# Performance work log

Measured on AMD Instinct MI355X. Metric: run time of the kernel, lower is better.

## Reference

```python
import jax, jax.numpy as jnp
import numpy as np

BATCH = 128
L = 4096
DIM = 64
N = 3   # rate-1/3 encoder: three 1-channel branches concatenated
EPS = 1e-3  # keras BatchNormalization default epsilon


def _bn(y, g, be, m, v):
    # inference-mode BatchNormalization over the channel (last) axis
    return g * (y - m) * jax.lax.rsqrt(v + EPS) + be


def _circ_unit(x, w, b, g, be, m, v):
    # Circular 'same' padding for kernel_size=5, stride=1 -> pad_window = 2
    xp = jnp.concatenate([x[:, -2:], x, x[:, :2]], axis=1)  # [B, L+4, C]
    y = jax.lax.conv_general_dilated(
        xp, w, window_strides=(1,), padding='VALID',
        dimension_numbers=('NWC', 'WIO', 'NWC')) + b        # [B, L, DIM]
    return jax.nn.elu(_bn(y, g, be, m, v))


def setup_inputs() -> dict:
    key = jax.random.key(0)
    ks = iter(jax.random.split(key, 16))

    def nrm(shape, s=0.05):
        return jax.random.normal(next(ks), shape, dtype=jnp.float32) * s

    inp = {}
    inp['x'] = jax.random.uniform(next(ks), (BATCH, L, 1), dtype=jnp.float32)
    # Pseudo_random_Interleaver: per-row permutation seeded by row index
    inp['perm'] = jnp.asarray(
        np.stack([np.random.RandomState(i).permutation(L) for i in range(BATCH)]),
        dtype=jnp.int32)
    for p in ('c1', 'c2', 'cI'):
        inp[p + '_w'] = nrm((5, 1, DIM)); inp[p + '_b'] = jnp.zeros((DIM,), jnp.float32)
        inp[p + '_g'] = jnp.ones((DIM,), jnp.float32); inp[p + '_be'] = jnp.zeros((DIM,), jnp.float32)
        inp[p + '_m'] = jnp.zeros((DIM,), jnp.float32); inp[p + '_v'] = jnp.ones((DIM,), jnp.float32)
    for p in ('f1', 'f2', 'fI'):
        inp[p + '_w'] = nrm((DIM, 1)); inp[p + '_b'] = jnp.zeros((1,), jnp.float32)
    inp['mp_w'] = nrm((1, DIM)); inp['mp_b'] = jnp.zeros((DIM,), jnp.float32)
    inp['mp_g'] = jnp.ones((DIM,), jnp.float32); inp['mp_be'] = jnp.zeros((DIM,), jnp.float32)
    inp['mp_m'] = jnp.zeros((DIM,), jnp.float32); inp['mp_v'] = jnp.ones((DIM,), jnp.float32)
    inp['md_w'] = nrm((DIM, 2)); inp['md_b'] = jnp.zeros((2,), jnp.float32)
    inp['md_g'] = jnp.ones((2,), jnp.float32); inp['md_be'] = jnp.zeros((2,), jnp.float32)
    inp['md_m'] = jnp.zeros((2,), jnp.float32); inp['md_v'] = jnp.ones((2,), jnp.float32)
    return inp


def reference(x, perm,
              c1_w, c1_b, c1_g, c1_be, c1_m, c1_v,
              c2_w, c2_b, c2_g, c2_be, c2_m, c2_v,
              cI_w, cI_b, cI_g, cI_be, cI_m, cI_v,
              f1_w, f1_b, f2_w, f2_b, fI_w, fI_b,
              mp_w, mp_b, mp_g, mp_be, mp_m, mp_v,
              md_w, md_b, md_g, md_be, md_m, md_v):
    x = 2.0 * x - 1.0  # bits -> +/-1
    # systematic branches
    e1 = jnp.einsum('bld,do->blo', _circ_unit(x, c1_w, c1_b, c1_g, c1_be, c1_m, c1_v), f1_w) + f1_b
    e2 = jnp.einsum('bld,do->blo', _circ_unit(x, c2_w, c2_b, c2_g, c2_be, c2_m, c2_v), f2_w) + f2_b
    # interleaved branch: one batched gather replaces the per-sample python loop
    xI = jnp.take_along_axis(x, perm[:, :, None], axis=1)
    eI = jnp.einsum('bld,do->blo', _circ_unit(xI, cI_w, cI_b, cI_g, cI_be, cI_m, cI_v), fI_w) + fI_b
    y = jnp.concatenate([e1, e2, eI], axis=-1)          # [B, L, 3]
    yt = y.reshape(BATCH, L * N, 1)                     # k = 1
    # Modulation: 1x1 conv (elu) then 1x1 conv to 2 coords (linear), each with BN
    mo = jax.nn.elu(_bn(jnp.einsum('blk,kd->bld', yt, mp_w) + mp_b, mp_g, mp_be, mp_m, mp_v))
    coord = _bn(jnp.einsum('bld,dc->blc', mo, md_w) + md_b, md_g, md_be, md_m, md_v)
    return coord  # [B, 3L, 2]
```

## Files before the change

### kernel.cpp

```cpp
#include <hip/hip_runtime.h>
#include <math.h>

#define BATCH 128
#define LL    4096
#define DIM   64
#define EPS   1e-3f
#define LUTN  2048

#define LOG2E 1.44269504088896340736f
#define LN2   0.69314718055994530942f

#define GC2 0.2402265069591007f
#define GC3 0.05550410866482158f
#define GC4 0.009618129107628477f
#define GC5 0.0013333558146428443f


typedef float f32x2 __attribute__((ext_vector_type(2)));

__device__ __forceinline__ f32x2 pk_fma(f32x2 a, f32x2 b, f32x2 c) {
    return __builtin_elementwise_fma(a, b, c);
}

__device__ __forceinline__ float elu_plain(float z) {
    return z > 0.0f ? z : (__expf(z) - 1.0f);
}

__global__ __launch_bounds__(256) void enc_prep(
    const float* __restrict__ cw0, const float* __restrict__ cb0, const float* __restrict__ cg0,
    const float* __restrict__ cbe0, const float* __restrict__ cm0, const float* __restrict__ cv0,
    const float* __restrict__ cw1, const float* __restrict__ cb1, const float* __restrict__ cg1,
    const float* __restrict__ cbe1, const float* __restrict__ cm1, const float* __restrict__ cv1,
    const float* __restrict__ cw2, const float* __restrict__ cb2, const float* __restrict__ cg2,
    const float* __restrict__ cbe2, const float* __restrict__ cm2, const float* __restrict__ cv2,
    const float* __restrict__ f0w, const float* __restrict__ f0b,
    const float* __restrict__ f1w, const float* __restrict__ f1b,
    const float* __restrict__ f2w, const float* __restrict__ f2b,
    const float* __restrict__ mpw, const float* __restrict__ mpb, const float* __restrict__ mpg,
    const float* __restrict__ mpbe, const float* __restrict__ mpm, const float* __restrict__ mpv,
    const float* __restrict__ mdw, const float* __restrict__ mdb, const float* __restrict__ mdg,
    const float* __restrict__ mdbe, const float* __restrict__ mdm, const float* __restrict__ mdv,
    float* __restrict__ W)
{
    const int t   = threadIdx.x;
    const int blk = blockIdx.x;
    __shared__ float smod[64][4];
    __shared__ float s_lo[3], s_hi[3];
    __shared__ float sD[2];
    __shared__ float srange[2];

    if (t < 192) {
        const int br = t >> 6;
        const int d  = t & 63;
        const float* cw  = (br == 0) ? cw0  : (br == 1) ? cw1  : cw2;
        const float* cb  = (br == 0) ? cb0  : (br == 1) ? cb1  : cb2;
        const float* cg  = (br == 0) ? cg0  : (br == 1) ? cg1  : cg2;
        const float* cbe = (br == 0) ? cbe0 : (br == 1) ? cbe1 : cbe2;
        const float* cm  = (br == 0) ? cm0  : (br == 1) ? cm1  : cm2;
        const float* cv  = (br == 0) ? cv0  : (br == 1) ? cv1  : cv2;
        const float* fw  = (br == 0) ? f0w  : (br == 1) ? f1w  : f2w;
        const float s = cg[d] / sqrtf(cv[d] + EPS);
        float tap[5], habs = 0.0f;
        #pragma unroll
        for (int k = 0; k < 5; ++k) {
            tap[k] = cw[k * 64 + d] * s * LOG2E;
            habs += fabsf(tap[k]);
        }
        const float bias = ((cb[d] - cm[d]) * s + cbe[d]) * LOG2E;
        const float fwd  = fw[d];
        if (blk == 0) {
            float* o = W + ((d >> 1) * 3 + br) * 16 + (d & 1);
            o[0] = tap[0]; o[2] = tap[1]; o[4] = tap[2]; o[6] = tap[3]; o[8] = tap[4];
            o[10] = bias; o[12] = fwd;
        }
        const float hb = LN2 * (habs + fabsf(bias));
        float r0 = fwd * tap[0], r1 = fwd * tap[1], r2 = fwd * tap[2];
        float r3 = fwd * tap[3], r4 = fwd * tap[4], rb = fwd * bias;
        float myS = fabsf(fwd) * fmaxf(1.0f, hb);
        #pragma unroll
        for (int off = 32; off; off >>= 1) {
            r0 += __shfl_down(r0, off);
            r1 += __shfl_down(r1, off);
            r2 += __shfl_down(r2, off);
            r3 += __shfl_down(r3, off);
            r4 += __shfl_down(r4, off);
            rb += __shfl_down(rb, off);
            myS += __shfl_down(myS, off);
        }
        if ((t & 63) == 0) {
            const float fb = ((br == 0) ? f0b : (br == 1) ? f1b : f2b)[0];
            s_lo[br] = fb - myS;
            s_hi[br] = fb + myS;
            if (blk == 0) {
                float* Lb = W + 1536 + br * 8;
                Lb[0] = LN2 * r0; Lb[1] = LN2 * r1; Lb[2] = LN2 * r2;
                Lb[3] = LN2 * r3; Lb[4] = LN2 * r4; Lb[5] = LN2 * rb;
                W[1560 + br] = fb;
            }
        }
    } else {
        const int d = t - 192;
        const float smp = mpg[d] / sqrtf(mpv[d] + EPS);
        const float A = mpw[d] * smp;
        const float C = (mpb[d] - mpm[d]) * smp + mpbe[d];
        const float s0 = mdg[0] / sqrtf(mdv[0] + EPS);
        const float s1 = mdg[1] / sqrtf(mdv[1] + EPS);
        smod[d][0] = A;
        smod[d][1] = C;
        smod[d][2] = mdw[d * 2 + 0] * s0;
        smod[d][3] = mdw[d * 2 + 1] * s1;
        if (d == 0) {
            const float D0 = (mdb[0] - mdm[0]) * s0 + mdbe[0];
            const float D1 = (mdb[1] - mdm[1]) * s1 + mdbe[1];
            sD[0] = D0; sD[1] = D1;
            if (blk == 0) { W[1563] = D0; W[1564] = D1; }
        }
    }
    __syncthreads();

    if (t == 0) {
        float lo = fminf(s_lo[0], fminf(s_lo[1], s_lo[2]));
        float hi = fmaxf(s_hi[0], fmaxf(s_hi[1], s_hi[2]));
        float pad = 1e-3f * (hi - lo) + 1e-6f;
        lo -= pad; hi += pad;
        srange[0] = lo;
        srange[1] = (hi - lo) / (float)(LUTN - 1);
        if (blk == 0) {
            const float invh = (float)(LUTN - 1) / (hi - lo);
            W[1565] = invh;
            W[1566] = -lo * invh;
            W[1567] = lo;
        }
    }
    __syncthreads();

    const int i = blk * 256 + t;
    const float lo = srange[0], hs = srange[1];
    const float D0 = sD[0], D1 = sD[1];
    const float e0 = fmaf((float)i, hs, lo);
    const float e1 = fmaf((float)(i + 1), hs, lo);
    float a0 = D0, a1 = D1, b0 = D0, b1 = D1;
    #pragma unroll 8
    for (int d = 0; d < 64; ++d) {
        const float A = smod[d][0], C = smod[d][1], m0 = smod[d][2], m1 = smod[d][3];
        float u;
        u = elu_plain(fmaf(A, e0, C)); a0 = fmaf(m0, u, a0); a1 = fmaf(m1, u, a1);
        u = elu_plain(fmaf(A, e1, C)); b0 = fmaf(m0, u, b0); b1 = fmaf(m1, u, b1);
    }
    float4* lut = (float4*)(W + 1568);
    lut[i] = make_float4(a0, a1, b0 - a0, b1 - a1);
}

__device__ __forceinline__ float2 lut_eval(float e, float invh, float nlo,
                                           const float4* __restrict__ lut) {
    float tt = fminf(fmaxf(fmaf(e, invh, nlo), 0.0f), (float)(LUTN - 1));
    float fi = floorf(tt); float f = tt - fi;
    float4 v = lut[(int)fi];
    return make_float2(fmaf(f, v.z, v.x), fmaf(f, v.w, v.y));
}

__device__ __forceinline__ void nl_acc(f32x2 h, f32x2 fw, f32x2& e) {
    const f32x2 zero = {0.0f, 0.0f};
    f32x2 z  = __builtin_elementwise_min(h, zero);
    f32x2 zz = z * z;
    f32x2 s  = pk_fma(z, f32x2{GC5, GC5}, f32x2{GC4, GC4});
    s = pk_fma(z, s, f32x2{GC3, GC3});
    s = pk_fma(z, s, f32x2{GC2, GC2});
    e = pk_fma(fw, zz * s, e);
}

__global__ __launch_bounds__(256) void enc_main(
    const float* __restrict__ x, const int* __restrict__ perm,
    const float* __restrict__ W, float* __restrict__ out)
{
    const int gid = blockIdx.x * 256 + threadIdx.x;
    const int b   = gid >> 11;
    const int l0  = (gid & (2048 - 1)) * 2;
    const float* xrow = x + ((size_t)b << 12);
    const int*   prow = perm + ((size_t)b << 12);

    const int ba = (l0 - 2) & (LL - 1);
    const int bc = (l0 + 2) & (LL - 1);
    const float2 w01 = *(const float2*)(xrow + ba);
    const float2 w23 = *(const float2*)(xrow + l0);
    const float2 w45 = *(const float2*)(xrow + bc);
    const int2 p01 = *(const int2*)(prow + ba);
    const int2 p23 = *(const int2*)(prow + l0);
    const int2 p45 = *(const int2*)(prow + bc);

    float xw[6], xg[6];
    xw[0] = fmaf(2.0f, w01.x, -1.0f); xw[1] = fmaf(2.0f, w01.y, -1.0f);
    xw[2] = fmaf(2.0f, w23.x, -1.0f); xw[3] = fmaf(2.0f, w23.y, -1.0f);
    xw[4] = fmaf(2.0f, w45.x, -1.0f); xw[5] = fmaf(2.0f, w45.y, -1.0f);
    xg[0] = fmaf(2.0f, xrow[p01.x], -1.0f); xg[1] = fmaf(2.0f, xrow[p01.y], -1.0f);
    xg[2] = fmaf(2.0f, xrow[p23.x], -1.0f); xg[3] = fmaf(2.0f, xrow[p23.y], -1.0f);
    xg[4] = fmaf(2.0f, xrow[p45.x], -1.0f); xg[5] = fmaf(2.0f, xrow[p45.y], -1.0f);

    f32x2 xs[6], xi[6];
    #pragma unroll
    for (int k = 0; k < 6; ++k) {
        xs[k] = f32x2{xw[k], xw[k]};
        xi[k] = f32x2{xg[k], xg[k]};
    }

    const float* LA = W + 1536;
    const float* LB = W + 1544;
    const float* LC = W + 1552;
    float linA0 = fmaf(LA[0], xw[0], fmaf(LA[1], xw[1], fmaf(LA[2], xw[2],
                  fmaf(LA[3], xw[3], fmaf(LA[4], xw[4], LA[5])))));
    float linA1 = fmaf(LA[0], xw[1], fmaf(LA[1], xw[2], fmaf(LA[2], xw[3],
                  fmaf(LA[3], xw[4], fmaf(LA[4], xw[5], LA[5])))));
    float linB0 = fmaf(LB[0], xw[0], fmaf(LB[1], xw[1], fmaf(LB[2], xw[2],
                  fmaf(LB[3], xw[3], fmaf(LB[4], xw[4], LB[5])))));
    float linB1 = fmaf(LB[0], xw[1], fmaf(LB[1], xw[2], fmaf(LB[2], xw[3],
                  fmaf(LB[3], xw[4], fmaf(LB[4], xw[5], LB[5])))));
    float linC0 = fmaf(LC[0], xg[0], fmaf(LC[1], xg[1], fmaf(LC[2], xg[2],
                  fmaf(LC[3], xg[3], fmaf(LC[4], xg[4], LC[5])))));
    float linC1 = fmaf(LC[0], xg[1], fmaf(LC[1], xg[2], fmaf(LC[2], xg[3],
                  fmaf(LC[3], xg[4], fmaf(LC[4], xg[5], LC[5])))));

    f32x2 eA0 = {0.0f, 0.0f}, eA1 = {0.0f, 0.0f};
    f32x2 eB0 = {0.0f, 0.0f}, eB1 = {0.0f, 0.0f};
    f32x2 eC0 = {0.0f, 0.0f}, eC1 = {0.0f, 0.0f};

    #pragma unroll 4
    for (int j = 0; j < 32; ++j) {
        const f32x2* tp = (const f32x2*)W + j * 24;
        f32x2 h;

        h = pk_fma(tp[0], xs[0], pk_fma(tp[1], xs[1], pk_fma(tp[2], xs[2],
            pk_fma(tp[3], xs[3], pk_fma(tp[4], xs[4], tp[5])))));
        nl_acc(h, tp[6], eA0);
        h = pk_fma(tp[0], xs[1], pk_fma(tp[1], xs[2], pk_fma(tp[2], xs[3],
            pk_fma(tp[3], xs[4], pk_fma(tp[4], xs[5], tp[5])))));
        nl_acc(h, tp[6], eA1);

        h = pk_fma(tp[8], xs[0], pk_fma(tp[9], xs[1], pk_fma(tp[10], xs[2],
            pk_fma(tp[11], xs[3], pk_fma(tp[12], xs[4], tp[13])))));
        nl_acc(h, tp[14], eB0);
        h = pk_fma(tp[8], xs[1], pk_fma(tp[9], xs[2], pk_fma(tp[10], xs[3],
            pk_fma(tp[11], xs[4], pk_fma(tp[12], xs[5], tp[13])))));
        nl_acc(h, tp[14], eB1);

        h = pk_fma(tp[16], xi[0], pk_fma(tp[17], xi[1], pk_fma(tp[18], xi[2],
            pk_fma(tp[19], xi[3], pk_fma(tp[20], xi[4], tp[21])))));
        nl_acc(h, tp[22], eC0);
        h = pk_fma(tp[16], xi[1], pk_fma(tp[17], xi[2], pk_fma(tp[18], xi[3],
            pk_fma(tp[19], xi[4], pk_fma(tp[20], xi[5], tp[21])))));
        nl_acc(h, tp[22], eC1);
    }

    const float fbA = W[1560], fbB = W[1561], fbC = W[1562];
    const float sA0 = fbA + linA0 + eA0.x + eA0.y;
    const float sA1 = fbA + linA1 + eA1.x + eA1.y;
    const float sB0 = fbB + linB0 + eB0.x + eB0.y;
    const float sB1 = fbB + linB1 + eB1.x + eB1.y;
    const float sC0 = fbC + linC0 + eC0.x + eC0.y;
    const float sC1 = fbC + linC1 + eC1.x + eC1.y;

    const float invh = W[1565], nlo = W[1566];
    const float4* lut = (const float4*)(W + 1568);
    float2 r0 = lut_eval(sA0, invh, nlo, lut);
    float2 r1 = lut_eval(sB0, invh, nlo, lut);
    float2 r2 = lut_eval(sC0, invh, nlo, lut);
    float2 r3 = lut_eval(sA1, invh, nlo, lut);
    float2 r4 = lut_eval(sB1, invh, nlo, lut);
    float2 r5 = lut_eval(sC1, invh, nlo, lut);

    float4* o4 = (float4*)(out + (size_t)gid * 12);
    o4[0] = make_float4(r0.x, r0.y, r1.x, r1.y);
    o4[1] = make_float4(r2.x, r2.y, r3.x, r3.y);
    o4[2] = make_float4(r4.x, r4.y, r5.x, r5.y);
}

extern "C" void kernel_launch(void* const* d_in, const int* in_sizes, int n_in,
                              void* d_out, int out_size, void* d_ws, size_t ws_size,
                              hipStream_t stream) {
    const float* x    = (const float*)d_in[0];
    const int*   perm = (const int*)d_in[1];
    float* W = (float*)d_ws;

    enc_prep<<<LUTN / 256, 256, 0, stream>>>(
        (const float*)d_in[2],  (const float*)d_in[3],  (const float*)d_in[4],
        (const float*)d_in[5],  (const float*)d_in[6],  (const float*)d_in[7],
        (const float*)d_in[8],  (const float*)d_in[9],  (const float*)d_in[10],
        (const float*)d_in[11], (const float*)d_in[12], (const float*)d_in[13],
        (const float*)d_in[14], (const float*)d_in[15], (const float*)d_in[16],
        (const float*)d_in[17], (const float*)d_in[18], (const float*)d_in[19],
        (const float*)d_in[20], (const float*)d_in[21],
        (const float*)d_in[22], (const float*)d_in[23],
        (const float*)d_in[24], (const float*)d_in[25],
        (const float*)d_in[26], (const float*)d_in[27], (const float*)d_in[28],
        (const float*)d_in[29], (const float*)d_in[30], (const float*)d_in[31],
        (const float*)d_in[32], (const float*)d_in[33], (const float*)d_in[34],
        (const float*)d_in[35], (const float*)d_in[36], (const float*)d_in[37],
        W);

    enc_main<<<(BATCH * LL) / 512, 256, 0, stream>>>(x, perm, W, (float*)d_out);
}
```

Before: 35.69 us.

## Process four positions per thread and fold x-to-bipolar mapping into weights

Each thread now computes four sequence positions instead of two. Weight loads from the workspace are amortized over twice as many conv and nonlinearity evaluations, and x/perm reads become float4/int4. The 2x-1 input transform is folded into the prepared taps, biases and linear terms, which removes the per-element FMA. The trade-off is higher register pressure, half as many threads and blocks (512 blocks), and the loop unroll dropping from 4 to 2.

```diff
diff --git a/kernel.cpp b/kernel.cpp
--- a/kernel.cpp
+++ b/kernel.cpp
@@ -60,18 +60,21 @@
         const float* cv  = (br == 0) ? cv0  : (br == 1) ? cv1  : cv2;
         const float* fw  = (br == 0) ? f0w  : (br == 1) ? f1w  : f2w;
         const float s = cg[d] / sqrtf(cv[d] + EPS);
-        float tap[5], habs = 0.0f;
+        float tap[5], habs = 0.0f, tsum = 0.0f;
         #pragma unroll
         for (int k = 0; k < 5; ++k) {
             tap[k] = cw[k * 64 + d] * s * LOG2E;
             habs += fabsf(tap[k]);
+            tsum += tap[k];
         }
         const float bias = ((cb[d] - cm[d]) * s + cbe[d]) * LOG2E;
         const float fwd  = fw[d];
         if (blk == 0) {
-            float* o = W + ((d >> 1) * 3 + br) * 16 + (d & 1);
-            o[0] = tap[0]; o[2] = tap[1]; o[4] = tap[2]; o[6] = tap[3]; o[8] = tap[4];
-            o[10] = bias; o[12] = fwd;
+            float* o = W + ((d >> 1) * 24 + br * 8) * 2 + (d & 1);
+            o[0] = 2.0f * tap[0]; o[2] = 2.0f * tap[1]; o[4] = 2.0f * tap[2];
+            o[6] = 2.0f * tap[3]; o[8] = 2.0f * tap[4];
+            o[10] = bias - tsum;
+            o[12] = fwd;
         }
         const float hb = LN2 * (habs + fabsf(bias));
         float r0 = fwd * tap[0], r1 = fwd * tap[1], r2 = fwd * tap[2];
@@ -93,8 +96,11 @@
             s_hi[br] = fb + myS;
             if (blk == 0) {
                 float* Lb = W + 1536 + br * 8;
-                Lb[0] = LN2 * r0; Lb[1] = LN2 * r1; Lb[2] = LN2 * r2;
-                Lb[3] = LN2 * r3; Lb[4] = LN2 * r4; Lb[5] = LN2 * rb;
+                const float rs = r0 + r1 + r2 + r3 + r4;
+                Lb[0] = 2.0f * LN2 * r0; Lb[1] = 2.0f * LN2 * r1;
+                Lb[2] = 2.0f * LN2 * r2; Lb[3] = 2.0f * LN2 * r3;
+                Lb[4] = 2.0f * LN2 * r4;
+                Lb[5] = LN2 * (rb - rs);
                 W[1560 + br] = fb;
             }
         }
@@ -169,108 +175,140 @@
     e = pk_fma(fw, zz * s, e);
 }
 
+#define CONV(tpb, xa, o) \
+    pk_fma(tpb[0], xa[o], pk_fma(tpb[1], xa[o+1], pk_fma(tpb[2], xa[o+2], \
+    pk_fma(tpb[3], xa[o+3], pk_fma(tpb[4], xa[o+4], tpb[5])))))
+
 __global__ __launch_bounds__(256) void enc_main(
     const float* __restrict__ x, const int* __restrict__ perm,
     const float* __restrict__ W, float* __restrict__ out)
 {
     const int gid = blockIdx.x * 256 + threadIdx.x;
-    const int b   = gid >> 11;
-    const int l0  = (gid & (2048 - 1)) * 2;
+    const int b   = gid >> 10;
+    const int l0  = (gid & 1023) * 4;
     const float* xrow = x + ((size_t)b << 12);
     const int*   prow = perm + ((size_t)b << 12);
 
-    const int ba = (l0 - 2) & (LL - 1);
-    const int bc = (l0 + 2) & (LL - 1);
-    const float2 w01 = *(const float2*)(xrow + ba);
-    const float2 w23 = *(const float2*)(xrow + l0);
-    const float2 w45 = *(const float2*)(xrow + bc);
-    const int2 p01 = *(const int2*)(prow + ba);
-    const int2 p23 = *(const int2*)(prow + l0);
-    const int2 p45 = *(const int2*)(prow + bc);
-
-    float xw[6], xg[6];
-    xw[0] = fmaf(2.0f, w01.x, -1.0f); xw[1] = fmaf(2.0f, w01.y, -1.0f);
-    xw[2] = fmaf(2.0f, w23.x, -1.0f); xw[3] = fmaf(2.0f, w23.y, -1.0f);
-    xw[4] = fmaf(2.0f, w45.x, -1.0f); xw[5] = fmaf(2.0f, w45.y, -1.0f);
-    xg[0] = fmaf(2.0f, xrow[p01.x], -1.0f); xg[1] = fmaf(2.0f, xrow[p01.y], -1.0f);
-    xg[2] = fmaf(2.0f, xrow[p23.x], -1.0f); xg[3] = fmaf(2.0f, xrow[p23.y], -1.0f);
-    xg[4] = fmaf(2.0f, xrow[p45.x], -1.0f); xg[5] = fmaf(2.0f, xrow[p45.y], -1.0f);
-
-    f32x2 xs[6], xi[6];
-    #pragma unroll
-    for (int k = 0; k < 6; ++k) {
-        xs[k] = f32x2{xw[k], xw[k]};
-        xi[k] = f32x2{xg[k], xg[k]};
-    }
+    const float4 q0 = *(const float4*)(xrow + ((l0 - 4) & (LL - 1)));
+    const float4 q1 = *(const float4*)(xrow + l0);
+    const float4 q2 = *(const float4*)(xrow + ((l0 + 4) & (LL - 1)));
+    const int4 pq0 = *(const int4*)(prow + ((l0 - 4) & (LL - 1)));
+    const int4 pq1 = *(const int4*)(prow + l0);
+    const int4 pq2 = *(const int4*)(prow + ((l0 + 4) & (LL - 1)));
+
+    float xw[8], xg[8];
+    xw[0] = q0.z; xw[1] = q0.w;
+    xw[2] = q1.x; xw[3] = q1.y; xw[4] = q1.z; xw[5] = q1.w;
+    xw[6] = q2.x; xw[7] = q2.y;
+    xg[0] = xrow[pq0.z]; xg[1] = xrow[pq0.w];
+    xg[2] = xrow[pq1.x]; xg[3] = xrow[pq1.y];
+    xg[4] = xrow[pq1.z]; xg[5] = xrow[pq1.w];
+    xg[6] = xrow[pq2.x]; xg[7] = xrow[pq2.y];
 
     const float* LA = W + 1536;
     const float* LB = W + 1544;
     const float* LC = W + 1552;
-    float linA0 = fmaf(LA[0], xw[0], fmaf(LA[1], xw[1], fmaf(LA[2], xw[2],
-                  fmaf(LA[3], xw[3], fmaf(LA[4], xw[4], LA[5])))));
-    float linA1 = fmaf(LA[0], xw[1], fmaf(LA[1], xw[2], fmaf(LA[2], xw[3],
-                  fmaf(LA[3], xw[4], fmaf(LA[4], xw[5], LA[5])))));
-    float linB0 = fmaf(LB[0], xw[0], fmaf(LB[1], xw[1], fmaf(LB[2], xw[2],
-                  fmaf(LB[3], xw[3], fmaf(LB[4], xw[4], LB[5])))));
-    float linB1 = fmaf(LB[0], xw[1], fmaf(LB[1], xw[2], fmaf(LB[2], xw[3],
-                  fmaf(LB[3], xw[4], fmaf(LB[4], xw[5], LB[5])))));
-    float linC0 = fmaf(LC[0], xg[0], fmaf(LC[1], xg[1], fmaf(LC[2], xg[2],
-                  fmaf(LC[3], xg[3], fmaf(LC[4], xg[4], LC[5])))));
-    float linC1 = fmaf(LC[0], xg[1], fmaf(LC[1], xg[2], fmaf(LC[2], xg[3],
-                  fmaf(LC[3], xg[4], fmaf(LC[4], xg[5], LC[5])))));
-
-    f32x2 eA0 = {0.0f, 0.0f}, eA1 = {0.0f, 0.0f};
-    f32x2 eB0 = {0.0f, 0.0f}, eB1 = {0.0f, 0.0f};
-    f32x2 eC0 = {0.0f, 0.0f}, eC1 = {0.0f, 0.0f};
-
-    #pragma unroll 4
+    f32x2 pw0[5], pw2[5], pg0[5], pg2[5];
+    #pragma unroll
+    for (int k = 0; k < 5; ++k) {
+        pw0[k] = f32x2{xw[k],     xw[k + 1]};
+        pw2[k] = f32x2{xw[k + 2], xw[k + 3]};
+        pg0[k] = f32x2{xg[k],     xg[k + 1]};
+        pg2[k] = f32x2{xg[k + 2], xg[k + 3]};
+    }
+    f32x2 linA01, linA23, linB01, linB23, linC01, linC23;
+    {
+        f32x2 la[6], lb[6], lc[6];
+        #pragma unroll
+        for (int k = 0; k < 6; ++k) {
+            la[k] = f32x2{LA[k], LA[k]};
+            lb[k] = f32x2{LB[k], LB[k]};
+            lc[k] = f32x2{LC[k], LC[k]};
+        }
+        linA01 = pk_fma(la[0], pw0[0], pk_fma(la[1], pw0[1], pk_fma(la[2], pw0[2],
+                 pk_fma(la[3], pw0[3], pk_fma(la[4], pw0[4], la[5])))));
+        linA23 = pk_fma(la[0], pw2[0], pk_fma(la[1], pw2[1], pk_fma(la[2], pw2[2],
+                 pk_fma(la[3], pw2[3], pk_fma(la[4], pw2[4], la[5])))));
+        linB01 = pk_fma(lb[0], pw0[0], pk_fma(lb[1], pw0[1], pk_fma(lb[2], pw0[2],
+                 pk_fma(lb[3], pw0[3], pk_fma(lb[4], pw0[4], lb[5])))));
+        linB23 = pk_fma(lb[0], pw2[0], pk_fma(lb[1], pw2[1], pk_fma(lb[2], pw2[2],
+                 pk_fma(lb[3], pw2[3], pk_fma(lb[4], pw2[4], lb[5])))));
+        linC01 = pk_fma(lc[0], pg0[0], pk_fma(lc[1], pg0[1], pk_fma(lc[2], pg0[2],
+                 pk_fma(lc[3], pg0[3], pk_fma(lc[4], pg0[4], lc[5])))));
+        linC23 = pk_fma(lc[0], pg2[0], pk_fma(lc[1], pg2[1], pk_fma(lc[2], pg2[2],
+                 pk_fma(lc[3], pg2[3], pk_fma(lc[4], pg2[4], lc[5])))));
+    }
+
+    f32x2 xs[8], xi[8];
+    #pragma unroll
+    for (int k = 0; k < 8; ++k) {
+        xs[k] = f32x2{xw[k], xw[k]};
+        xi[k] = f32x2{xg[k], xg[k]};
+    }
+
+    f32x2 eA0 = {0, 0}, eA1 = {0, 0}, eA2 = {0, 0}, eA3 = {0, 0};
+    f32x2 eB0 = {0, 0}, eB1 = {0, 0}, eB2 = {0, 0}, eB3 = {0, 0};
+    f32x2 eC0 = {0, 0}, eC1 = {0, 0}, eC2 = {0, 0}, eC3 = {0, 0};
+
+    #pragma unroll 2
     for (int j = 0; j < 32; ++j) {
         const f32x2* tp = (const f32x2*)W + j * 24;
-        f32x2 h;
-
-        h = pk_fma(tp[0], xs[0], pk_fma(tp[1], xs[1], pk_fma(tp[2], xs[2],
-            pk_fma(tp[3], xs[3], pk_fma(tp[4], xs[4], tp[5])))));
-        nl_acc(h, tp[6], eA0);
-        h = pk_fma(tp[0], xs[1], pk_fma(tp[1], xs[2], pk_fma(tp[2], xs[3],
-            pk_fma(tp[3], xs[4], pk_fma(tp[4], xs[5], tp[5])))));
-        nl_acc(h, tp[6], eA1);
-
-        h = pk_fma(tp[8], xs[0], pk_fma(tp[9], xs[1], pk_fma(tp[10], xs[2],
-            pk_fma(tp[11], xs[3], pk_fma(tp[12], xs[4], tp[13])))));
-        nl_acc(h, tp[14], eB0);
-        h = pk_fma(tp[8], xs[1], pk_fma(tp[9], xs[2], pk_fma(tp[10], xs[3],
-            pk_fma(tp[11], xs[4], pk_fma(tp[12], xs[5], tp[13])))));
-        nl_acc(h, tp[14], eB1);
-
-        h = pk_fma(tp[16], xi[0], pk_fma(tp[17], xi[1], pk_fma(tp[18], xi[2],
-            pk_fma(tp[19], xi[3], pk_fma(tp[20], xi[4], tp[21])))));
-        nl_acc(h, tp[22], eC0);
-        h = pk_fma(tp[16], xi[1], pk_fma(tp[17], xi[2], pk_fma(tp[18], xi[3],
-            pk_fma(tp[19], xi[4], pk_fma(tp[20], xi[5], tp[21])))));
-        nl_acc(h, tp[22], eC1);
+        const f32x2* t0 = tp;
+        const f32x2* t1 = tp + 8;
+        const f32x2* t2 = tp + 16;
+
+        nl_acc(CONV(t0, xs, 0), t0[6], eA0);
+        nl_acc(CONV(t0, xs, 1), t0[6], eA1);
+        nl_acc(CONV(t0, xs, 2), t0[6], eA2);
+        nl_acc(CONV(t0, xs, 3), t0[6], eA3);
+
+        nl_acc(CONV(t1, xs, 0), t1[6], eB0);
+        nl_acc(CONV(t1, xs, 1), t1[6], eB1);
+        nl_acc(CONV(t1, xs, 2), t1[6], eB2);
+        nl_acc(CONV(t1, xs, 3), t1[6], eB3);
+
+        nl_acc(CONV(t2, xi, 0), t2[6], eC0);
+        nl_acc(CONV(t2, xi, 1), t2[6], eC1);
+        nl_acc(CONV(t2, xi, 2), t2[6], eC2);
+        nl_acc(CONV(t2, xi, 3), t2[6], eC3);
     }
 
     const float fbA = W[1560], fbB = W[1561], fbC = W[1562];
-    const float sA0 = fbA + linA0 + eA0.x + eA0.y;
-    const float sA1 = fbA + linA1 + eA1.x + eA1.y;
-    const float sB0 = fbB + linB0 + eB0.x + eB0.y;
-    const float sB1 = fbB + linB1 + eB1.x + eB1.y;
-    const float sC0 = fbC + linC0 + eC0.x + eC0.y;
-    const float sC1 = fbC + linC1 + eC1.x + eC1.y;
+    const float sA0 = fbA + linA01.x + eA0.x + eA0.y;
+    const float sA1 = fbA + linA01.y + eA1.x + eA1.y;
+    const float sA2 = fbA + linA23.x + eA2.x + eA2.y;
+    const float sA3 = fbA + linA23.y + eA3.x + eA3.y;
+    const float sB0 = fbB + linB01.x + eB0.x + eB0.y;
+    const float sB1 = fbB + linB01.y + eB1.x + eB1.y;
+    const float sB2 = fbB + linB23.x + eB2.x + eB2.y;
+    const float sB3 = fbB + linB23.y + eB3.x + eB3.y;
+    const float sC0 = fbC + linC01.x + eC0.x + eC0.y;
+    const float sC1 = fbC + linC01.y + eC1.x + eC1.y;
+    const float sC2 = fbC + linC23.x + eC2.x + eC2.y;
+    const float sC3 = fbC + linC23.y + eC3.x + eC3.y;
 
     const float invh = W[1565], nlo = W[1566];
     const float4* lut = (const float4*)(W + 1568);
-    float2 r0 = lut_eval(sA0, invh, nlo, lut);
-    float2 r1 = lut_eval(sB0, invh, nlo, lut);
-    float2 r2 = lut_eval(sC0, invh, nlo, lut);
-    float2 r3 = lut_eval(sA1, invh, nlo, lut);
-    float2 r4 = lut_eval(sB1, invh, nlo, lut);
-    float2 r5 = lut_eval(sC1, invh, nlo, lut);
-
-    float4* o4 = (float4*)(out + (size_t)gid * 12);
-    o4[0] = make_float4(r0.x, r0.y, r1.x, r1.y);
-    o4[1] = make_float4(r2.x, r2.y, r3.x, r3.y);
-    o4[2] = make_float4(r4.x, r4.y, r5.x, r5.y);
+    float2 rA0 = lut_eval(sA0, invh, nlo, lut);
+    float2 rB0 = lut_eval(sB0, invh, nlo, lut);
+    float2 rC0 = lut_eval(sC0, invh, nlo, lut);
+    float2 rA1 = lut_eval(sA1, invh, nlo, lut);
+    float2 rB1 = lut_eval(sB1, invh, nlo, lut);
+    float2 rC1 = lut_eval(sC1, invh, nlo, lut);
+    float2 rA2 = lut_eval(sA2, invh, nlo, lut);
+    float2 rB2 = lut_eval(sB2, invh, nlo, lut);
+    float2 rC2 = lut_eval(sC2, invh, nlo, lut);
+    float2 rA3 = lut_eval(sA3, invh, nlo, lut);
+    float2 rB3 = lut_eval(sB3, invh, nlo, lut);
+    float2 rC3 = lut_eval(sC3, invh, nlo, lut);
+
+    float4* o4 = (float4*)(out + (size_t)gid * 24);
+    o4[0] = make_float4(rA0.x, rA0.y, rB0.x, rB0.y);
+    o4[1] = make_float4(rC0.x, rC0.y, rA1.x, rA1.y);
+    o4[2] = make_float4(rB1.x, rB1.y, rC1.x, rC1.y);
+    o4[3] = make_float4(rA2.x, rA2.y, rB2.x, rB2.y);
+    o4[4] = make_float4(rC2.x, rC2.y, rA3.x, rA3.y);
+    o4[5] = make_float4(rB3.x, rB3.y, rC3.x, rC3.y);
 }
 
 extern "C" void kernel_launch(void* const* d_in, const int* in_sizes, int n_in,
@@ -296,5 +334,5 @@
         (const float*)d_in[35], (const float*)d_in[36], (const float*)d_in[37],
         W);
 
-    enc_main<<<(BATCH * LL) / 512, 256, 0, stream>>>(x, perm, W, (float*)d_out);
-}
+    enc_main<<<(BATCH * LL) / 1024, 256, 0, stream>>>(x, perm, W, (float*)d_out);
+}
```

Result: slower. 39.10 us (+9.6%).
